# Performance work log

Hardware: AMD Instinct MI355X
Metric: run time of the kernel (lower is better)

The kernel has to match this reference:

```python
import jax, jax.numpy as jnp
import numpy as np

N = 50000        # total nodes (disjoint batch of graphs)
E = 800000       # total edges
F_IN = 8         # node feature dim
S = 6            # edge feature dim
H = 20           # ECC kernel-network hidden size (hidden_states)
N_OUT = 20       # ECC output channels (n_out=hidden_states)
G = 32           # GCN channels
D1 = 16          # first dense
N_GRAPHS = 512   # graphs in batch


def setup_inputs() -> dict:
    key = jax.random.key(0)
    ks = jax.random.split(key, 24)
    r = lambda k, sh, s: jax.random.normal(k, sh, dtype=jnp.float32) * s
    return {
        "x": r(ks[0], (N, F_IN), 1.0),
        "e": r(ks[1], (E, S), 1.0),
        "edge_index": jax.random.randint(ks[2], (2, E), 0, N, dtype=jnp.int32),
        "seg": jnp.sort(jax.random.randint(ks[3], (N,), 0, N_GRAPHS, dtype=jnp.int32)),
        # ECC kernel network: S -> H -> H -> F_IN*N_OUT
        "ecc_w1": r(ks[4], (S, H), 0.4), "ecc_b1": jnp.zeros((H,), jnp.float32),
        "ecc_w2": r(ks[5], (H, H), 0.2), "ecc_b2": jnp.zeros((H,), jnp.float32),
        "ecc_w3": r(ks[6], (H, F_IN * N_OUT), 0.2), "ecc_b3": jnp.zeros((F_IN * N_OUT,), jnp.float32),
        "ecc_root": r(ks[7], (F_IN, N_OUT), 0.3), "ecc_b": jnp.zeros((N_OUT,), jnp.float32),
        "gcn1_w": r(ks[8], (N_OUT, G), 0.2), "gcn1_b": jnp.zeros((G,), jnp.float32),
        "gcn2_w": r(ks[9], (G, G), 0.2), "gcn2_b": jnp.zeros((G,), jnp.float32),
        "d1_w": r(ks[10], (G, D1), 0.2), "d1_b": jnp.zeros((D1,), jnp.float32),
        "d2_w": r(ks[11], (D1, 1), 0.2), "d2_b": jnp.zeros((1,), jnp.float32),
    }


def reference(x, e, edge_index, seg,
              ecc_w1, ecc_b1, ecc_w2, ecc_b2, ecc_w3, ecc_b3, ecc_root, ecc_b,
              gcn1_w, gcn1_b, gcn2_w, gcn2_b, d1_w, d1_b, d2_w, d2_b):
    row, col = edge_index[0], edge_index[1]  # message col -> row

    # --- ECCConv: per-edge MLP produces an [F_IN, N_OUT] filter per edge ---
    h = jax.nn.relu(e @ ecc_w1 + ecc_b1)
    h = jax.nn.relu(h @ ecc_w2 + ecc_b2)
    w_edge = (h @ ecc_w3 + ecc_b3).reshape(E, F_IN, N_OUT)   # [E, F_in, F_out]
    msg = jnp.einsum('ef,efo->eo', x[col], w_edge)            # per-edge message
    agg = jax.ops.segment_sum(msg, row, num_segments=N)
    x1 = jax.nn.relu(agg + x @ ecc_root + ecc_b)              # root + bias + relu

    # --- GCN normalization from the edge list (A + I, symmetric norm) ---
    deg = jax.ops.segment_sum(jnp.ones((E,), x.dtype), row, num_segments=N) + 1.0
    dinv = jax.lax.rsqrt(deg)
    edge_norm = (dinv[row] * dinv[col])[:, None]
    self_norm = (dinv * dinv)[:, None]

    def gcn(hin, W, b):
        hw = hin @ W
        nmsg = jax.ops.segment_sum(edge_norm * hw[col], row, num_segments=N)
        return jax.nn.relu(nmsg + self_norm * hw + b)

    x2 = gcn(x1, gcn1_w, gcn1_b)
    x3 = gcn(x2, gcn2_w, gcn2_b)

    # --- GlobalSumPool over graph ids, then MLP head ---
    pooled = jax.ops.segment_sum(x3, seg, num_segments=N_GRAPHS)  # [n_graphs, G]
    out = (pooled @ d1_w + d1_b) @ d2_w + d2_b                    # [n_graphs, 1]
    return out
```

## Files before the change

kernel.cpp:

```cpp
#include <hip/hip_runtime.h>

#define S_DIM   6
#define H_DIM   20
#define F_INN   8
#define N_OUTC  20
#define G_DIM   32
#define D1_DIM  16
#define NGRAPH  512

__global__ __launch_bounds__(256) void loc_kernel(
    const int* __restrict__ ei, int E, int* __restrict__ cnt,
    int* __restrict__ loc)
{
    int i = blockIdx.x * 256 + threadIdx.x;
    if (i >= E) return;
    loc[i] = atomicAdd(&cnt[ei[i]], 1);
}

__global__ __launch_bounds__(256) void scanA_kernel(
    const int* __restrict__ deg, int N, int* __restrict__ bsum)
{
    int i = blockIdx.x * 256 + threadIdx.x;
    int v = (i < N) ? deg[i] : 0;
#pragma unroll
    for (int d = 1; d < 64; d <<= 1) v += __shfl_down(v, d, 64);
    __shared__ int ws[4];
    int wid = threadIdx.x >> 6;
    if ((threadIdx.x & 63) == 0) ws[wid] = v;
    __syncthreads();
    if (threadIdx.x == 0) bsum[blockIdx.x] = ws[0] + ws[1] + ws[2] + ws[3];
}

__global__ __launch_bounds__(256) void scanB_kernel(
    const int* __restrict__ bsum, int nb, int E,
    int* __restrict__ boff, int* __restrict__ rowptr, int N)
{
    int t = threadIdx.x;
    int v = (t < nb) ? bsum[t] : 0;
    int orig = v;
#pragma unroll
    for (int d = 1; d < 64; d <<= 1) {
        int u = __shfl_up(v, d, 64);
        if ((t & 63) >= d) v += u;
    }
    __shared__ int ws[4];
    int wid = t >> 6;
    if ((t & 63) == 63) ws[wid] = v;
    __syncthreads();
    int woff = 0;
    for (int w = 0; w < wid; ++w) woff += ws[w];
    if (t < nb) boff[t] = woff + v - orig;
    if (t == 0) rowptr[N] = E;
}

__global__ __launch_bounds__(256) void scanC_kernel(
    const int* __restrict__ deg, int N, const int* __restrict__ boff,
    int* __restrict__ rowptr, float* __restrict__ dinv)
{
    int i = blockIdx.x * 256 + threadIdx.x;
    int t = threadIdx.x;
    int d0 = (i < N) ? deg[i] : 0;
    int v = d0;
#pragma unroll
    for (int d = 1; d < 64; d <<= 1) {
        int u = __shfl_up(v, d, 64);
        if ((t & 63) >= d) v += u;
    }
    __shared__ int ws[4];
    int wid = t >> 6;
    if ((t & 63) == 63) ws[wid] = v;
    __syncthreads();
    int woff = 0;
    for (int w = 0; w < wid; ++w) woff += ws[w];
    if (i < N) {
        rowptr[i] = boff[blockIdx.x] + woff + v - d0;
        dinv[i] = rsqrtf((float)d0 + 1.0f);
    }
}

__global__ __launch_bounds__(256) void build_kernel(
    const int* __restrict__ ei, int E, const int* __restrict__ rowptr,
    const int* __restrict__ loc,
    int* __restrict__ eid_at_slot, int* __restrict__ col_sorted)
{
    int i = blockIdx.x * 256 + threadIdx.x;
    if (i >= E) return;
    int p = rowptr[ei[i]] + loc[i];
    eid_at_slot[p] = i;
    col_sorted[p] = ei[E + i];
}

__global__ __launch_bounds__(256) void ecc_fused_kernel(
    const float* __restrict__ e, const float* __restrict__ x,
    const int* __restrict__ eid_at_slot, const int* __restrict__ col_sorted,
    const int* __restrict__ rowptr, int N, int E,
    const float* __restrict__ w1, const float* __restrict__ b1,
    const float* __restrict__ w2, const float* __restrict__ b2,
    const float* __restrict__ w3, const float* __restrict__ b3,
    float* __restrict__ agg)
{
    __shared__ float4 lmsg[5][256];
    __shared__ int rbounds[2];

    int t = threadIdx.x;
    int j0 = blockIdx.x * 256;
    int j = j0 + t;
    int jend = min(j0 + 256, E);

    if (t < 2) {
        int s = (t == 0) ? j0 : (jend - 1);
        int lo = 0, hi = N - 1;
        while (lo < hi) {
            int m = (lo + hi + 1) >> 1;
            if (rowptr[m] <= s) lo = m; else hi = m - 1;
        }
        rbounds[t] = lo;
    }

    if (j < E) {
        int i = eid_at_slot[j];
        int c = col_sorted[j];

        float ef[S_DIM];
#pragma unroll
        for (int s = 0; s < S_DIM; ++s) ef[s] = e[(size_t)i * S_DIM + s];

        float h1[H_DIM];
#pragma unroll
        for (int jj = 0; jj < H_DIM; ++jj) {
            float a = b1[jj];
#pragma unroll
            for (int s = 0; s < S_DIM; ++s) a = fmaf(ef[s], w1[s * H_DIM + jj], a);
            h1[jj] = fmaxf(a, 0.0f);
        }

        float h2[H_DIM];
#pragma unroll
        for (int jj = 0; jj < H_DIM; ++jj) {
            float a = b2[jj];
#pragma unroll
            for (int k = 0; k < H_DIM; ++k) a = fmaf(h1[k], w2[k * H_DIM + jj], a);
            h2[jj] = fmaxf(a, 0.0f);
        }

        const float4* xp = (const float4*)&x[(size_t)c * F_INN];
        float4 xa = xp[0], xb = xp[1];
        float xf[F_INN] = {xa.x, xa.y, xa.z, xa.w, xb.x, xb.y, xb.z, xb.w};

        float msg[N_OUTC];
#pragma unroll
        for (int o = 0; o < N_OUTC; ++o) msg[o] = 0.0f;

        for (int f = 0; f < F_INN; ++f) {
            float xv = xf[f];
#pragma unroll
            for (int o = 0; o < N_OUTC; ++o) {
                float w = b3[f * N_OUTC + o];
#pragma unroll
                for (int k = 0; k < H_DIM; ++k)
                    w = fmaf(h2[k], w3[k * (F_INN * N_OUTC) + f * N_OUTC + o], w);
                msg[o] = fmaf(xv, w, msg[o]);
            }
        }

        lmsg[0][t] = make_float4(msg[0],  msg[1],  msg[2],  msg[3]);
        lmsg[1][t] = make_float4(msg[4],  msg[5],  msg[6],  msg[7]);
        lmsg[2][t] = make_float4(msg[8],  msg[9],  msg[10], msg[11]);
        lmsg[3][t] = make_float4(msg[12], msg[13], msg[14], msg[15]);
        lmsg[4][t] = make_float4(msg[16], msg[17], msg[18], msg[19]);
    }
    __syncthreads();

    int r0 = rbounds[0], r1 = rbounds[1];
    int work = (r1 - r0 + 1) * 5;
    for (int w = t; w < work; w += 256) {
        int row = r0 + w / 5;
        int q = w - (w / 5) * 5;
        int a0 = rowptr[row], a1 = rowptr[row + 1];
        int s0 = max(a0, j0), s1 = min(a1, jend);
        float4 acc = make_float4(0.f, 0.f, 0.f, 0.f);
        for (int s = s0; s < s1; ++s) {
            float4 v = lmsg[q][s - j0];
            acc.x += v.x; acc.y += v.y; acc.z += v.z; acc.w += v.w;
        }
        float* dst = &agg[(size_t)row * N_OUTC + q * 4];
        if (a0 >= j0 && a1 <= jend) {
            *(float4*)dst = acc;
        } else {
            unsafeAtomicAdd(dst + 0, acc.x);
            unsafeAtomicAdd(dst + 1, acc.y);
            unsafeAtomicAdd(dst + 2, acc.z);
            unsafeAtomicAdd(dst + 3, acc.w);
        }
    }
}

__global__ __launch_bounds__(256) void node1_kernel(
    const float* __restrict__ agg, const float* __restrict__ x, int N,
    const float* __restrict__ root, const float* __restrict__ eb,
    const float* __restrict__ g1w,
    float* __restrict__ hw1)
{
    int n = blockIdx.x * 256 + threadIdx.x;
    if (n >= N) return;

    const float4* xp = (const float4*)&x[(size_t)n * F_INN];
    float4 xa = xp[0], xb = xp[1];
    float xf[F_INN] = {xa.x, xa.y, xa.z, xa.w, xb.x, xb.y, xb.z, xb.w};

    float x1[N_OUTC];
#pragma unroll
    for (int o = 0; o < N_OUTC; ++o) {
        float a = agg[(size_t)n * N_OUTC + o] + eb[o];
#pragma unroll
        for (int f = 0; f < F_INN; ++f) a = fmaf(xf[f], root[f * N_OUTC + o], a);
        x1[o] = fmaxf(a, 0.0f);
    }

    float4* hp = (float4*)&hw1[(size_t)n * G_DIM];
#pragma unroll
    for (int q = 0; q < G_DIM / 4; ++q) {
        float4 v;
        float* vv = &v.x;
#pragma unroll
        for (int u = 0; u < 4; ++u) {
            int g = q * 4 + u;
            float a = 0.0f;
#pragma unroll
            for (int o = 0; o < N_OUTC; ++o) a = fmaf(x1[o], g1w[o * G_DIM + g], a);
            vv[u] = a;
        }
        hp[q] = v;
    }
}

template<bool DO_MATMUL>
__global__ __launch_bounds__(256) void gcn_gather_kernel(
    const float* __restrict__ hw, const int* __restrict__ rowptr,
    const int* __restrict__ col_sorted, const float* __restrict__ dinv, int N,
    const float* __restrict__ bias, const float* __restrict__ w2,
    float* __restrict__ outbuf)
{
    __shared__ float x2s[32 * 33];
    __shared__ float w2s[G_DIM * G_DIM];

    int t = threadIdx.x;
    int nl = t >> 3;
    int q = t & 7;
    int n = blockIdx.x * 32 + nl;

    if (DO_MATMUL) {
        ((float4*)w2s)[t] = ((const float4*)w2)[t];
    }

    float4 xo = make_float4(0.f, 0.f, 0.f, 0.f);
    if (n < N) {
        int j0 = rowptr[n], j1 = rowptr[n + 1];
        float4 s = make_float4(0.f, 0.f, 0.f, 0.f);
        for (int j = j0; j < j1; ++j) {
            int c = col_sorted[j];
            float w = dinv[c];
            float4 v = *(const float4*)&hw[(size_t)c * G_DIM + q * 4];
            s.x = fmaf(w, v.x, s.x);
            s.y = fmaf(w, v.y, s.y);
            s.z = fmaf(w, v.z, s.z);
            s.w = fmaf(w, v.w, s.w);
        }
        float di = dinv[n];
        float sn = di * di;
        float4 self = *(const float4*)&hw[(size_t)n * G_DIM + q * 4];
        const float4 b4 = *(const float4*)&bias[q * 4];
        xo.x = fmaxf(fmaf(di, s.x, fmaf(sn, self.x, b4.x)), 0.0f);
        xo.y = fmaxf(fmaf(di, s.y, fmaf(sn, self.y, b4.y)), 0.0f);
        xo.z = fmaxf(fmaf(di, s.z, fmaf(sn, self.z, b4.z)), 0.0f);
        xo.w = fmaxf(fmaf(di, s.w, fmaf(sn, self.w, b4.w)), 0.0f);
    }

    if (DO_MATMUL) {
        x2s[nl * 33 + q * 4 + 0] = xo.x;
        x2s[nl * 33 + q * 4 + 1] = xo.y;
        x2s[nl * 33 + q * 4 + 2] = xo.z;
        x2s[nl * 33 + q * 4 + 3] = xo.w;
        __syncthreads();
        if (n < N) {
            float a0 = 0.f, a1 = 0.f, a2 = 0.f, a3 = 0.f;
            const float* xr = &x2s[nl * 33];
#pragma unroll
            for (int g = 0; g < G_DIM; ++g) {
                float xv = xr[g];
                a0 = fmaf(xv, w2s[g * G_DIM + q * 4 + 0], a0);
                a1 = fmaf(xv, w2s[g * G_DIM + q * 4 + 1], a1);
                a2 = fmaf(xv, w2s[g * G_DIM + q * 4 + 2], a2);
                a3 = fmaf(xv, w2s[g * G_DIM + q * 4 + 3], a3);
            }
            *(float4*)&outbuf[(size_t)n * G_DIM + q * 4] = make_float4(a0, a1, a2, a3);
        }
    } else {
        if (n < N)
            *(float4*)&outbuf[(size_t)n * G_DIM + q * 4] = xo;
    }
}

__global__ __launch_bounds__(256) void pool_kernel(
    const float* __restrict__ x3, const int* __restrict__ seg, int N,
    float* __restrict__ pooled)
{
    __shared__ float red[8][G_DIM];
    __shared__ int bounds[2];
    int g = blockIdx.x;
    int t = threadIdx.x;
    if (t < 2) {
        int target = g + t;
        int lo = 0, hi = N;
        while (lo < hi) {
            int m = (lo + hi) >> 1;
            if (seg[m] < target) lo = m + 1; else hi = m;
        }
        bounds[t] = lo;
    }
    __syncthreads();
    int n0 = bounds[0], n1 = bounds[1];
    int ch = t & (G_DIM - 1);
    int slice = t >> 5;
    float a = 0.0f;
    for (int n = n0 + slice; n < n1; n += 8)
        a += x3[(size_t)n * G_DIM + ch];
    red[slice][ch] = a;
    __syncthreads();
    if (slice == 0) {
        float s = red[0][ch];
#pragma unroll
        for (int k = 1; k < 8; ++k) s += red[k][ch];
        pooled[g * G_DIM + ch] = s;
    }
}

__global__ __launch_bounds__(256) void head_kernel(
    const float* __restrict__ pooled,
    const float* __restrict__ d1w, const float* __restrict__ d1b,
    const float* __restrict__ d2w, const float* __restrict__ d2b,
    float* __restrict__ out)
{
    int i = blockIdx.x * 256 + threadIdx.x;
    if (i >= NGRAPH) return;

    float p[G_DIM];
#pragma unroll
    for (int g = 0; g < G_DIM; ++g) p[g] = pooled[i * G_DIM + g];

    float acc = d2b[0];
#pragma unroll
    for (int j = 0; j < D1_DIM; ++j) {
        float t = d1b[j];
#pragma unroll
        for (int g = 0; g < G_DIM; ++g) t = fmaf(p[g], d1w[g * D1_DIM + j], t);
        acc = fmaf(t, d2w[j], acc);
    }
    out[i] = acc;
}

extern "C" void kernel_launch(void* const* d_in, const int* in_sizes, int n_in,
                              void* d_out, int out_size, void* d_ws, size_t ws_size,
                              hipStream_t stream)
{
    const float* x    = (const float*)d_in[0];
    const float* e    = (const float*)d_in[1];
    const int*   ei   = (const int*)d_in[2];
    const int*   seg  = (const int*)d_in[3];
    const float* w1   = (const float*)d_in[4];
    const float* b1   = (const float*)d_in[5];
    const float* w2   = (const float*)d_in[6];
    const float* b2   = (const float*)d_in[7];
    const float* w3   = (const float*)d_in[8];
    const float* b3   = (const float*)d_in[9];
    const float* root = (const float*)d_in[10];
    const float* eb   = (const float*)d_in[11];
    const float* g1w  = (const float*)d_in[12];
    const float* g1b  = (const float*)d_in[13];
    const float* g2w  = (const float*)d_in[14];
    const float* g2b  = (const float*)d_in[15];
    const float* d1w  = (const float*)d_in[16];
    const float* d1b  = (const float*)d_in[17];
    const float* d2w  = (const float*)d_in[18];
    const float* d2b  = (const float*)d_in[19];

    const int N = in_sizes[3];
    const int E = in_sizes[1] / S_DIM;
    float* out = (float*)d_out;

    const int nbl = (N + 255) / 256;
    const int ebl = (E + 255) / 256;

    char* ws = (char*)d_ws;
    size_t off = 0;
    auto alloc = [&](size_t elems) -> char* {
        char* p = ws + off;
        off += ((elems * 4 + 15) & ~(size_t)15);
        return p;
    };
    int*   cnt        = (int*)  alloc(N);
    float* agg        = (float*)alloc((size_t)N * N_OUTC);
    size_t zero_bytes = off;
    int*   rowptr     = (int*)  alloc(N + 1);
    int*   bsum       = (int*)  alloc(nbl);
    int*   boff       = (int*)  alloc(nbl);
    float* dinv       = (float*)alloc(N);
    int*   loc        = (int*)  alloc(E);
    int*   eid_at_slot= (int*)  alloc(E);
    int*   col_sorted = (int*)  alloc(E);
    float* hw1        = (float*)alloc((size_t)N * G_DIM);
    float* hw2        = (float*)alloc((size_t)N * G_DIM);
    float* x3         = (float*)alloc((size_t)N * G_DIM);
    float* pooled     = (float*)alloc((size_t)NGRAPH * G_DIM);
    (void)ws_size;

    hipMemsetAsync(d_ws, 0, zero_bytes, stream);

    loc_kernel<<<ebl, 256, 0, stream>>>(ei, E, cnt, loc);
    scanA_kernel<<<nbl, 256, 0, stream>>>(cnt, N, bsum);
    scanB_kernel<<<1, 256, 0, stream>>>(bsum, nbl, E, boff, rowptr, N);
    scanC_kernel<<<nbl, 256, 0, stream>>>(cnt, N, boff, rowptr, dinv);
    build_kernel<<<ebl, 256, 0, stream>>>(ei, E, rowptr, loc, eid_at_slot, col_sorted);
    ecc_fused_kernel<<<ebl, 256, 0, stream>>>(e, x, eid_at_slot, col_sorted,
                                              rowptr, N, E,
                                              w1, b1, w2, b2, w3, b3, agg);
    node1_kernel<<<nbl, 256, 0, stream>>>(agg, x, N, root, eb, g1w, hw1);
    gcn_gather_kernel<true><<<(N + 31) / 32, 256, 0, stream>>>(
        hw1, rowptr, col_sorted, dinv, N, g1b, g2w, hw2);
    gcn_gather_kernel<false><<<(N + 31) / 32, 256, 0, stream>>>(
        hw2, rowptr, col_sorted, dinv, N, g2b, nullptr, x3);
    pool_kernel<<<NGRAPH, 256, 0, stream>>>(x3, seg, N, pooled);
    head_kernel<<<(NGRAPH + 255) / 256, 256, 0, stream>>>(pooled, d1w, d1b, d2w, d2b, out);
}
```

Measured before the change: 324.9 us.

## Fold dinv scaling into producers, merge scan stages, fuse pool with head

Scales hw rows by dinv at the source (node1 and the GCN1 matmul epilogue), so the gather loop no longer loads dinv[col] per edge and the self term becomes the initial accumulator. Merges scanB into scanC: each block reduces the preceding block sums itself. Fuses the pool and head kernels, and pads the ECC shared buffer by one element. This removes two launches and a random per-edge load, at the cost of a redundant prefix reduction in every scan block.

After: 314.6 us. -3.2%, faster.

```diff
diff --git a/kernel.cpp b/kernel.cpp
--- a/kernel.cpp
+++ b/kernel.cpp
@@ -31,51 +31,44 @@
     if (threadIdx.x == 0) bsum[blockIdx.x] = ws[0] + ws[1] + ws[2] + ws[3];
 }
 
-__global__ __launch_bounds__(256) void scanB_kernel(
-    const int* __restrict__ bsum, int nb, int E,
-    int* __restrict__ boff, int* __restrict__ rowptr, int N)
-{
+__global__ __launch_bounds__(256) void scanC_kernel(
+    const int* __restrict__ deg, int N, const int* __restrict__ bsum, int nbl,
+    int E, int* __restrict__ rowptr, float* __restrict__ dinv)
+{
+    __shared__ int ws[4];
+    __shared__ int sboff;
     int t = threadIdx.x;
-    int v = (t < nb) ? bsum[t] : 0;
-    int orig = v;
+
+    {
+        int v = (t < nbl && t < blockIdx.x) ? bsum[t] : 0;
+#pragma unroll
+        for (int d = 1; d < 64; d <<= 1) v += __shfl_down(v, d, 64);
+        int wid = t >> 6;
+        if ((t & 63) == 0) ws[wid] = v;
+        __syncthreads();
+        if (t == 0) sboff = ws[0] + ws[1] + ws[2] + ws[3];
+        __syncthreads();
+    }
+
+    int i = blockIdx.x * 256 + t;
+    int d0 = (i < N) ? deg[i] : 0;
+    int v = d0;
 #pragma unroll
     for (int d = 1; d < 64; d <<= 1) {
         int u = __shfl_up(v, d, 64);
         if ((t & 63) >= d) v += u;
     }
-    __shared__ int ws[4];
+    __shared__ int ws2[4];
     int wid = t >> 6;
-    if ((t & 63) == 63) ws[wid] = v;
+    if ((t & 63) == 63) ws2[wid] = v;
     __syncthreads();
     int woff = 0;
-    for (int w = 0; w < wid; ++w) woff += ws[w];
-    if (t < nb) boff[t] = woff + v - orig;
-    if (t == 0) rowptr[N] = E;
-}
-
-__global__ __launch_bounds__(256) void scanC_kernel(
-    const int* __restrict__ deg, int N, const int* __restrict__ boff,
-    int* __restrict__ rowptr, float* __restrict__ dinv)
-{
-    int i = blockIdx.x * 256 + threadIdx.x;
-    int t = threadIdx.x;
-    int d0 = (i < N) ? deg[i] : 0;
-    int v = d0;
-#pragma unroll
-    for (int d = 1; d < 64; d <<= 1) {
-        int u = __shfl_up(v, d, 64);
-        if ((t & 63) >= d) v += u;
-    }
-    __shared__ int ws[4];
-    int wid = t >> 6;
-    if ((t & 63) == 63) ws[wid] = v;
-    __syncthreads();
-    int woff = 0;
-    for (int w = 0; w < wid; ++w) woff += ws[w];
+    for (int w = 0; w < wid; ++w) woff += ws2[w];
     if (i < N) {
-        rowptr[i] = boff[blockIdx.x] + woff + v - d0;
+        rowptr[i] = sboff + woff + v - d0;
         dinv[i] = rsqrtf((float)d0 + 1.0f);
     }
+    if (blockIdx.x == 0 && t == 0) rowptr[N] = E;
 }
 
 __global__ __launch_bounds__(256) void build_kernel(
@@ -99,7 +92,7 @@
     const float* __restrict__ w3, const float* __restrict__ b3,
     float* __restrict__ agg)
 {
-    __shared__ float4 lmsg[5][256];
+    __shared__ float4 lmsg[5][257];
     __shared__ int rbounds[2];
 
     int t = threadIdx.x;
@@ -196,10 +189,11 @@
 }
 
 __global__ __launch_bounds__(256) void node1_kernel(
-    const float* __restrict__ agg, const float* __restrict__ x, int N,
+    const float* __restrict__ agg, const float* __restrict__ x,
+    const float* __restrict__ dinv, int N,
     const float* __restrict__ root, const float* __restrict__ eb,
     const float* __restrict__ g1w,
-    float* __restrict__ hw1)
+    float* __restrict__ hws1)
 {
     int n = blockIdx.x * 256 + threadIdx.x;
     if (n >= N) return;
@@ -217,7 +211,8 @@
         x1[o] = fmaxf(a, 0.0f);
     }
 
-    float4* hp = (float4*)&hw1[(size_t)n * G_DIM];
+    float di = dinv[n];
+    float4* hp = (float4*)&hws1[(size_t)n * G_DIM];
 #pragma unroll
     for (int q = 0; q < G_DIM / 4; ++q) {
         float4 v;
@@ -228,7 +223,7 @@
             float a = 0.0f;
 #pragma unroll
             for (int o = 0; o < N_OUTC; ++o) a = fmaf(x1[o], g1w[o * G_DIM + g], a);
-            vv[u] = a;
+            vv[u] = a * di;
         }
         hp[q] = v;
     }
@@ -236,7 +231,7 @@
 
 template<bool DO_MATMUL>
 __global__ __launch_bounds__(256) void gcn_gather_kernel(
-    const float* __restrict__ hw, const int* __restrict__ rowptr,
+    const float* __restrict__ hws, const int* __restrict__ rowptr,
     const int* __restrict__ col_sorted, const float* __restrict__ dinv, int N,
     const float* __restrict__ bias, const float* __restrict__ w2,
     float* __restrict__ outbuf)
@@ -254,26 +249,21 @@
     }
 
     float4 xo = make_float4(0.f, 0.f, 0.f, 0.f);
+    float di = 0.0f;
     if (n < N) {
+        di = dinv[n];
         int j0 = rowptr[n], j1 = rowptr[n + 1];
-        float4 s = make_float4(0.f, 0.f, 0.f, 0.f);
+        float4 s = *(const float4*)&hws[(size_t)n * G_DIM + q * 4];
         for (int j = j0; j < j1; ++j) {
             int c = col_sorted[j];
-            float w = dinv[c];
-            float4 v = *(const float4*)&hw[(size_t)c * G_DIM + q * 4];
-            s.x = fmaf(w, v.x, s.x);
-            s.y = fmaf(w, v.y, s.y);
-            s.z = fmaf(w, v.z, s.z);
-            s.w = fmaf(w, v.w, s.w);
-        }
-        float di = dinv[n];
-        float sn = di * di;
-        float4 self = *(const float4*)&hw[(size_t)n * G_DIM + q * 4];
+            float4 v = *(const float4*)&hws[(size_t)c * G_DIM + q * 4];
+            s.x += v.x; s.y += v.y; s.z += v.z; s.w += v.w;
+        }
         const float4 b4 = *(const float4*)&bias[q * 4];
-        xo.x = fmaxf(fmaf(di, s.x, fmaf(sn, self.x, b4.x)), 0.0f);
-        xo.y = fmaxf(fmaf(di, s.y, fmaf(sn, self.y, b4.y)), 0.0f);
-        xo.z = fmaxf(fmaf(di, s.z, fmaf(sn, self.z, b4.z)), 0.0f);
-        xo.w = fmaxf(fmaf(di, s.w, fmaf(sn, self.w, b4.w)), 0.0f);
+        xo.x = fmaxf(fmaf(di, s.x, b4.x), 0.0f);
+        xo.y = fmaxf(fmaf(di, s.y, b4.y), 0.0f);
+        xo.z = fmaxf(fmaf(di, s.z, b4.z), 0.0f);
+        xo.w = fmaxf(fmaf(di, s.w, b4.w), 0.0f);
     }
 
     if (DO_MATMUL) {
@@ -293,7 +283,8 @@
                 a2 = fmaf(xv, w2s[g * G_DIM + q * 4 + 2], a2);
                 a3 = fmaf(xv, w2s[g * G_DIM + q * 4 + 3], a3);
             }
-            *(float4*)&outbuf[(size_t)n * G_DIM + q * 4] = make_float4(a0, a1, a2, a3);
+            *(float4*)&outbuf[(size_t)n * G_DIM + q * 4] =
+                make_float4(a0 * di, a1 * di, a2 * di, a3 * di);
         }
     } else {
         if (n < N)
@@ -301,11 +292,14 @@
     }
 }
 
-__global__ __launch_bounds__(256) void pool_kernel(
+__global__ __launch_bounds__(256) void pool_head_kernel(
     const float* __restrict__ x3, const int* __restrict__ seg, int N,
-    float* __restrict__ pooled)
+    const float* __restrict__ d1w, const float* __restrict__ d1b,
+    const float* __restrict__ d2w, const float* __restrict__ d2b,
+    float* __restrict__ out)
 {
     __shared__ float red[8][G_DIM];
+    __shared__ float pvec[G_DIM];
     __shared__ int bounds[2];
     int g = blockIdx.x;
     int t = threadIdx.x;
@@ -331,32 +325,19 @@
         float s = red[0][ch];
 #pragma unroll
         for (int k = 1; k < 8; ++k) s += red[k][ch];
-        pooled[g * G_DIM + ch] = s;
-    }
-}
-
-__global__ __launch_bounds__(256) void head_kernel(
-    const float* __restrict__ pooled,
-    const float* __restrict__ d1w, const float* __restrict__ d1b,
-    const float* __restrict__ d2w, const float* __restrict__ d2b,
-    float* __restrict__ out)
-{
-    int i = blockIdx.x * 256 + threadIdx.x;
-    if (i >= NGRAPH) return;
-
-    float p[G_DIM];
-#pragma unroll
-    for (int g = 0; g < G_DIM; ++g) p[g] = pooled[i * G_DIM + g];
-
-    float acc = d2b[0];
-#pragma unroll
-    for (int j = 0; j < D1_DIM; ++j) {
-        float t = d1b[j];
-#pragma unroll
-        for (int g = 0; g < G_DIM; ++g) t = fmaf(p[g], d1w[g * D1_DIM + j], t);
-        acc = fmaf(t, d2w[j], acc);
-    }
-    out[i] = acc;
+        pvec[ch] = s;
+    }
+    __syncthreads();
+    if (t < D1_DIM) {
+        float tj = d1b[t];
+#pragma unroll
+        for (int gg = 0; gg < G_DIM; ++gg)
+            tj = fmaf(pvec[gg], d1w[gg * D1_DIM + t], tj);
+        float acc = tj * d2w[t];
+#pragma unroll
+        for (int d = 1; d < D1_DIM; d <<= 1) acc += __shfl_down(acc, d, 64);
+        if (t == 0) out[g] = acc + d2b[0];
+    }
 }
 
 extern "C" void kernel_launch(void* const* d_in, const int* in_sizes, int n_in,
@@ -403,32 +384,28 @@
     size_t zero_bytes = off;
     int*   rowptr     = (int*)  alloc(N + 1);
     int*   bsum       = (int*)  alloc(nbl);
-    int*   boff       = (int*)  alloc(nbl);
     float* dinv       = (float*)alloc(N);
     int*   loc        = (int*)  alloc(E);
     int*   eid_at_slot= (int*)  alloc(E);
     int*   col_sorted = (int*)  alloc(E);
-    float* hw1        = (float*)alloc((size_t)N * G_DIM);
-    float* hw2        = (float*)alloc((size_t)N * G_DIM);
+    float* hws1       = (float*)alloc((size_t)N * G_DIM);
+    float* hws2       = (float*)alloc((size_t)N * G_DIM);
     float* x3         = (float*)alloc((size_t)N * G_DIM);
-    float* pooled     = (float*)alloc((size_t)NGRAPH * G_DIM);
     (void)ws_size;
 
     hipMemsetAsync(d_ws, 0, zero_bytes, stream);
 
     loc_kernel<<<ebl, 256, 0, stream>>>(ei, E, cnt, loc);
     scanA_kernel<<<nbl, 256, 0, stream>>>(cnt, N, bsum);
-    scanB_kernel<<<1, 256, 0, stream>>>(bsum, nbl, E, boff, rowptr, N);
-    scanC_kernel<<<nbl, 256, 0, stream>>>(cnt, N, boff, rowptr, dinv);
+    scanC_kernel<<<nbl, 256, 0, stream>>>(cnt, N, bsum, nbl, E, rowptr, dinv);
     build_kernel<<<ebl, 256, 0, stream>>>(ei, E, rowptr, loc, eid_at_slot, col_sorted);
     ecc_fused_kernel<<<ebl, 256, 0, stream>>>(e, x, eid_at_slot, col_sorted,
                                               rowptr, N, E,
                                               w1, b1, w2, b2, w3, b3, agg);
-    node1_kernel<<<nbl, 256, 0, stream>>>(agg, x, N, root, eb, g1w, hw1);
+    node1_kernel<<<nbl, 256, 0, stream>>>(agg, x, dinv, N, root, eb, g1w, hws1);
     gcn_gather_kernel<true><<<(N + 31) / 32, 256, 0, stream>>>(
-        hw1, rowptr, col_sorted, dinv, N, g1b, g2w, hw2);
+        hws1, rowptr, col_sorted, dinv, N, g1b, g2w, hws2);
     gcn_gather_kernel<false><<<(N + 31) / 32, 256, 0, stream>>>(
-        hw2, rowptr, col_sorted, dinv, N, g2b, nullptr, x3);
-    pool_kernel<<<NGRAPH, 256, 0, stream>>>(x3, seg, N, pooled);
-    head_kernel<<<(NGRAPH + 255) / 256, 256, 0, stream>>>(pooled, d1w, d1b, d2w, d2b, out);
-}
+        hws2, rowptr, col_sorted, dinv, N, g2b, nullptr, x3);
+    pool_head_kernel<<<NGRAPH, 256, 0, stream>>>(x3, seg, N, d1w, d1b, d2w, d2b, out);
+}
```
